# Kernel optimization log

Measured on AMD Instinct MI355X. Metric: run time of the kernel, lower is better.

## Reference

```python
import jax, jax.numpy as jnp
import numpy as np
from jax import lax

B, CIN, COUT, H, W = 8, 256, 256, 96, 96


def _conv_bn(x, w, g, b, act):
    # 3x3 conv, stride 1, SAME padding (NCHW / OIHW), then per-channel affine (folded BN)
    y = lax.conv_general_dilated(x, w, (1, 1), 'SAME',
                                 dimension_numbers=('NCHW', 'OIHW', 'NCHW'))
    y = y * g[None, :, None, None] + b[None, :, None, None]
    return jax.nn.relu(y) if act else y


def setup_inputs() -> dict:
    key = jax.random.key(0)
    ks = jax.random.split(key, 16)
    def wgt(k, cout, cin):
        return jax.random.normal(k, (cout, cin, 3, 3), jnp.float32) * (1.0 / np.sqrt(cin * 9))
    def gb(k, c):
        k1, k2 = jax.random.split(k)
        return (1.0 + 0.1 * jax.random.normal(k1, (c,), jnp.float32),
                0.1 * jax.random.normal(k2, (c,), jnp.float32))
    g_p1, b_p1 = gb(ks[1], COUT); g_p2, b_p2 = gb(ks[3], COUT)
    g_p, b_p = gb(ks[5], COUT); g_c1, b_c1 = gb(ks[7], COUT); g_c2, b_c2 = gb(ks[9], COUT)
    return {
        'x': jax.random.normal(ks[0], (B, CIN, H, W), jnp.float32),
        'w_p1': wgt(ks[10], COUT, CIN), 'g_p1': g_p1, 'b_p1': b_p1,
        'w_p2': wgt(ks[11], COUT, CIN), 'g_p2': g_p2, 'b_p2': b_p2,
        'w_p': wgt(ks[12], COUT, COUT), 'g_p': g_p, 'b_p': b_p,
        'w_c1': wgt(ks[13], COUT, CIN), 'g_c1': g_c1, 'b_c1': b_c1,
        'w_c2': wgt(ks[14], COUT, COUT), 'g_c2': g_c2, 'b_c2': b_c2,
    }


def reference(x, w_p1, g_p1, b_p1, w_p2, g_p2, b_p2, w_p, g_p, b_p,
              w_c1, g_c1, b_c1, w_c2, g_c2, b_c2):
    # branch 1: conv -> TopPool (cummax up, i.e. reverse along H) -> BottomPool (cummax down)
    p1 = _conv_bn(x, w_p1, g_p1, b_p1, act=True)
    pool1 = lax.cummax(p1, axis=2, reverse=True)   # TopPool
    pool1 = lax.cummax(pool1, axis=2)              # BottomPool
    # branch 2: conv -> LeftPool (reverse along W) -> RightPool
    p2 = _conv_bn(x, w_p2, g_p2, b_p2, act=True)
    pool2 = lax.cummax(p2, axis=3, reverse=True)   # LeftPool
    pool2 = lax.cummax(pool2, axis=3)              # RightPool
    p_conv = _conv_bn(pool1 + pool2, w_p, g_p, b_p, act=False)
    conv1 = _conv_bn(x, w_c1, g_c1, b_c1, act=False)
    relu = jax.nn.relu(p_conv + conv1)
    return _conv_bn(relu, w_c2, g_c2, b_c2, act=True)
```

## Files before the change

### kernel.cpp

```cpp
#include <hip/hip_runtime.h>


typedef _Float16 f16x8 __attribute__((ext_vector_type(8)));
typedef _Float16 f16x4v __attribute__((ext_vector_type(4)));
typedef float f32x4 __attribute__((ext_vector_type(4)));

#define HP 98
#define WP 98
#define KTOT 2304
#define WSET (256*KTOT)
#define XPAD_E ((size_t)8*HP*WP*256)
#define UVP_E  ((size_t)8*98*256)
#define UV2_E  ((size_t)3*8*96*256)
#define WUV_SET 196608

__device__ __forceinline__ int xcd_swz(int bid, int nwg)
{
  return (bid & 7) * (nwg >> 3) + (bid >> 3);
}

#define BUF_Q 24576
#define SMEM_Q 49152

struct CtxQ {
  unsigned goff[6];
  unsigned lds_stage;
  unsigned aoff;
  int wl, quad, wv;
  int b, h0, w0;
};

template<int SW>
__device__ __forceinline__ CtxQ make_ctxQ(int spatial, int ch)
{
  CtxQ c;
  c.b = spatial / 36;
  const int tt = spatial - c.b * 36;
  const int ht = tt / 6, wt = tt - ht * 6;
  c.h0 = ht * 16; c.w0 = wt * 16;
  const int tid = threadIdx.x, lane = tid & 63;
  c.wv = tid >> 6;
  c.quad = lane >> 4; c.wl = lane & 15;
  c.aoff = (unsigned)((ch * 8 + c.wv * 2) * 512 + c.wl * 32 + c.quad * 8);
  const unsigned base_hw = (unsigned)(c.b * HP + c.h0) * WP + c.w0;
#pragma unroll
  for (int t = 0; t < 6; ++t) {
    int s = (c.wv * 6 + t) * 16 + (lane >> 2);
    if (s > 323) s = 323;
    const int x = s / 18, y = s - x * 18;
    const int wh = SW ? y : x, ww = SW ? x : y;
    c.goff[t] = (base_hw + (unsigned)(wh * WP + ww)) * 256u + (lane & 3) * 8u;
  }
  c.lds_stage = (unsigned)(c.wv * 6) * 1024u + (unsigned)lane * 16u;
  return c;
}

__device__ __forceinline__ void stage_cbQ(const _Float16* __restrict__ src,
                                          char* sbuf, const CtxQ& c, int buf, int cb)
{
  char* l0 = sbuf + buf * BUF_Q + c.lds_stage;
#pragma unroll
  for (int t = 0; t < 6; ++t) {
    const _Float16* g = src + c.goff[t] + cb * 32;
    __builtin_amdgcn_global_load_lds(
        (const __attribute__((address_space(1))) void*)g,
        (__attribute__((address_space(3))) void*)(l0 + t * 1024), 16, 0, 0);
  }
}

template<int TR>
__device__ __forceinline__ void conv_accumQ(const _Float16* __restrict__ src,
                                            const _Float16* __restrict__ wkb,
                                            char* sbuf, const CtxQ& c, f32x4 acc[2][16])
{
  const _Float16* A0 = wkb + c.aoff;
  stage_cbQ(src, sbuf, c, 0, 0);
#pragma unroll 1
  for (int cb = 0; cb < 8; ++cb) {
    __syncthreads();
    if (cb < 7) stage_cbQ(src, sbuf, c, (cb + 1) & 1, cb + 1);
    const _Float16* B = (const _Float16*)(sbuf + (cb & 1) * BUF_Q);
    const _Float16* A = A0 + cb * (9 * 8192);
#pragma unroll
    for (int o = 0; o < 3; ++o) {
      f16x8 af[3][2];
#pragma unroll
      for (int p = 0; p < 3; ++p) {
        const int tap = (TR == 0) ? p * 3 + o : o * 3 + p;
#pragma unroll
        for (int i = 0; i < 2; ++i)
          af[p][i] = *(const f16x8*)(A + tap * 8192 + i * 512);
      }
#pragma unroll
      for (int jh = 0; jh < 2; ++jh) {
        f16x8 cache[10];
#pragma unroll
        for (int r = 0; r < 10; ++r)
          cache[r] = *(const f16x8*)(B + ((jh * 8 + r) * 18 + c.wl + o) * 32 + c.quad * 8);
#pragma unroll
        for (int p = 0; p < 3; ++p)
#pragma unroll
          for (int i = 0; i < 2; ++i)
#pragma unroll
            for (int j = 0; j < 8; ++j)
              acc[i][jh * 8 + j] = __builtin_amdgcn_mfma_f32_16x16x32_f16(
                  af[p][i], cache[j + p], acc[i][jh * 8 + j], 0, 0, 0);
      }
    }
  }
  __syncthreads();
}

#define ZERO_ACCQ(acc) \
  _Pragma("unroll") for (int i = 0; i < 2; ++i) \
  _Pragma("unroll") for (int j = 0; j < 16; ++j) acc[i][j] = (f32x4){0.f,0.f,0.f,0.f};

__global__ __launch_bounds__(256, 2) void k_conv_p12(
    const _Float16* __restrict__ xpad, const _Float16* __restrict__ wk,
    const float* __restrict__ bias1, const float* __restrict__ bias2,
    float* __restrict__ u_pad, float* __restrict__ v_pad)
{
  __shared__ __align__(16) char smem[SMEM_Q];
  const int lin = xcd_swz(blockIdx.x, 1152);
  const int set = lin >= 576;
  const int rem = lin - set * 576;
  const int spatial = rem >> 1, ch = rem & 1;
  f32x4 acc[2][16];
  ZERO_ACCQ(acc)
  if (set == 0) {
    CtxQ c = make_ctxQ<0>(spatial, ch);
    conv_accumQ<0>(xpad, wk, smem, c, acc);
#pragma unroll
    for (int i = 0; i < 2; ++i) {
      const int co = (ch * 8 + c.wv * 2 + i) * 16 + c.quad * 4;
      const float4 bs = *(const float4*)(bias1 + co);
      float m0 = 0.f, m1 = 0.f, m2 = 0.f, m3 = 0.f;
#pragma unroll
      for (int j = 0; j < 16; ++j) {
        m0 = fmaxf(m0, acc[i][j][0] + bs.x);
        m1 = fmaxf(m1, acc[i][j][1] + bs.y);
        m2 = fmaxf(m2, acc[i][j][2] + bs.z);
        m3 = fmaxf(m3, acc[i][j][3] + bs.w);
      }
      unsigned* tgt = (unsigned*)(u_pad + ((size_t)c.b * 98 + (c.w0 + c.wl + 1)) * 256 + co);
      atomicMax(tgt + 0, __float_as_uint(m0));
      atomicMax(tgt + 1, __float_as_uint(m1));
      atomicMax(tgt + 2, __float_as_uint(m2));
      atomicMax(tgt + 3, __float_as_uint(m3));
    }
  } else {
    CtxQ c = make_ctxQ<1>(spatial, ch);
    conv_accumQ<1>(xpad, wk + WSET, smem, c, acc);
#pragma unroll
    for (int i = 0; i < 2; ++i) {
      const int co = (ch * 8 + c.wv * 2 + i) * 16 + c.quad * 4;
      const float4 bs = *(const float4*)(bias2 + co);
      float m0 = 0.f, m1 = 0.f, m2 = 0.f, m3 = 0.f;
#pragma unroll
      for (int j = 0; j < 16; ++j) {
        m0 = fmaxf(m0, acc[i][j][0] + bs.x);
        m1 = fmaxf(m1, acc[i][j][1] + bs.y);
        m2 = fmaxf(m2, acc[i][j][2] + bs.z);
        m3 = fmaxf(m3, acc[i][j][3] + bs.w);
      }
      unsigned* tgt = (unsigned*)(v_pad + ((size_t)c.b * 98 + (c.h0 + c.wl + 1)) * 256 + co);
      atomicMax(tgt + 0, __float_as_uint(m0));
      atomicMax(tgt + 1, __float_as_uint(m1));
      atomicMax(tgt + 2, __float_as_uint(m2));
      atomicMax(tgt + 3, __float_as_uint(m3));
    }
  }
}

__global__ __launch_bounds__(256, 2) void k_uv1d(
    const float* __restrict__ u_pad, const float* __restrict__ v_pad,
    const _Float16* __restrict__ wuv, float* __restrict__ u2, float* __restrict__ v2)
{
  const int id = blockIdx.x;
  const int b = id & 7, cs = (id >> 3) % 3, t = id / 24;
  const float* src = t ? v_pad : u_pad;
  float* dst = t ? v2 : u2;
  const _Float16* A0 = wuv + (size_t)(t * 3 + cs) * WUV_SET;
  const int lane = threadIdx.x & 63, wv = threadIdx.x >> 6;
  const int quad = lane >> 4, l16 = lane & 15;

  f32x4 acc[4][6];
#pragma unroll
  for (int i = 0; i < 4; ++i)
#pragma unroll
    for (int j = 0; j < 6; ++j) acc[i][j] = (f32x4){0.f, 0.f, 0.f, 0.f};

#pragma unroll 1
  for (int kb = 0; kb < 24; ++kb) {
    const int dw = kb >> 3, cb = kb & 7;
    f16x8 bf[6];
#pragma unroll
    for (int j = 0; j < 6; ++j) {
      const int pos = j * 16 + l16;
      const float* p = src + ((size_t)b * 98 + (pos + dw)) * 256 + cb * 32 + quad * 8;
      const float4 x0 = *(const float4*)p;
      const float4 x1 = *(const float4*)(p + 4);
      f16x8 v;
      v[0] = (_Float16)x0.x; v[1] = (_Float16)x0.y; v[2] = (_Float16)x0.z; v[3] = (_Float16)x0.w;
      v[4] = (_Float16)x1.x; v[5] = (_Float16)x1.y; v[6] = (_Float16)x1.z; v[7] = (_Float16)x1.w;
      bf[j] = v;
    }
    f16x8 af[4];
#pragma unroll
    for (int i = 0; i < 4; ++i)
      af[i] = *(const f16x8*)(A0 + (size_t)(kb * 16 + wv * 4 + i) * 512 + l16 * 32 + quad * 8);
#pragma unroll
    for (int i = 0; i < 4; ++i)
#pragma unroll
      for (int j = 0; j < 6; ++j)
        acc[i][j] = __builtin_amdgcn_mfma_f32_16x16x32_f16(af[i], bf[j], acc[i][j], 0, 0, 0);
  }
#pragma unroll
  for (int i = 0; i < 4; ++i)
#pragma unroll
    for (int j = 0; j < 6; ++j) {
      const int pos = j * 16 + l16;
      const int co = wv * 64 + i * 16 + quad * 4;
      *(f32x4*)(dst + ((size_t)(cs * 8 + b) * 96 + pos) * 256 + co) = acc[i][j];
    }
}

__global__ __launch_bounds__(256, 2) void k_conv_c1f(
    const _Float16* __restrict__ xpad, const _Float16* __restrict__ wkc1,
    const float* __restrict__ bias_p, const float* __restrict__ bias_c1,
    const float* __restrict__ u2, const float* __restrict__ v2,
    _Float16* __restrict__ rpad)
{
  __shared__ __align__(16) char smem[SMEM_Q];
  const int lin = xcd_swz(blockIdx.x, 576);
  const int spatial = lin >> 1, ch = lin & 1;
  CtxQ c = make_ctxQ<0>(spatial, ch);
  f32x4 acc[2][16];
  ZERO_ACCQ(acc)
  conv_accumQ<0>(xpad, wkc1, smem, c, acc);

  const int w = c.w0 + c.wl;
  const int wcase = (w == 0) ? 0 : ((w == 95) ? 2 : 1);
#pragma unroll
  for (int i = 0; i < 2; ++i) {
    const int co = (ch * 8 + c.wv * 2 + i) * 16 + c.quad * 4;
    float4 bs = *(const float4*)(bias_p + co);
    const float4 b2 = *(const float4*)(bias_c1 + co);
    bs.x += b2.x; bs.y += b2.y; bs.z += b2.z; bs.w += b2.w;
#pragma unroll
    for (int j = 0; j < 16; ++j) {
      const int h = c.h0 + j;
      const int hcase = (h == 0) ? 0 : ((h == 95) ? 2 : 1);
      const float4 uq = *(const float4*)(u2 + ((size_t)(hcase * 8 + c.b) * 96 + w) * 256 + co);
      const float4 vq = *(const float4*)(v2 + ((size_t)(wcase * 8 + c.b) * 96 + h) * 256 + co);
      f16x4v pk;
      pk[0] = (_Float16)fmaxf(acc[i][j][0] + bs.x + uq.x + vq.x, 0.f);
      pk[1] = (_Float16)fmaxf(acc[i][j][1] + bs.y + uq.y + vq.y, 0.f);
      pk[2] = (_Float16)fmaxf(acc[i][j][2] + bs.z + uq.z + vq.z, 0.f);
      pk[3] = (_Float16)fmaxf(acc[i][j][3] + bs.w + uq.w + vq.w, 0.f);
      *(f16x4v*)(rpad + ((size_t)(c.b * HP + h + 1) * WP + w + 1) * 256 + co) = pk;
    }
  }
}

__global__ __launch_bounds__(256, 2) void k_conv_c2(
    const _Float16* __restrict__ rpad, const _Float16* __restrict__ wkc2,
    const float* __restrict__ bias, float* __restrict__ dout)
{
  __shared__ __align__(16) char smem[SMEM_Q];
  const int lin = xcd_swz(blockIdx.x, 576);
  const int spatial = lin >> 1, ch = lin & 1;
  CtxQ c = make_ctxQ<0>(spatial, ch);
  f32x4 acc[2][16];
  ZERO_ACCQ(acc)
  conv_accumQ<0>(rpad, wkc2, smem, c, acc);

  const int w = c.w0 + c.wl;
#pragma unroll
  for (int j = 0; j < 16; ++j) {
    const int h = c.h0 + j;
    float* op = dout + (size_t)c.b * 2359296 + h * 96 + w;
#pragma unroll
    for (int i = 0; i < 2; ++i) {
      const int co = (ch * 8 + c.wv * 2 + i) * 16 + c.quad * 4;
      const float4 bs = *(const float4*)(bias + co);
      op[(size_t)(co + 0) * 9216] = fmaxf(acc[i][j][0] + bs.x, 0.f);
      op[(size_t)(co + 1) * 9216] = fmaxf(acc[i][j][1] + bs.y, 0.f);
      op[(size_t)(co + 2) * 9216] = fmaxf(acc[i][j][2] + bs.z, 0.f);
      op[(size_t)(co + 3) * 9216] = fmaxf(acc[i][j][3] + bs.w, 0.f);
    }
  }
}

__global__ void k_border(_Float16* __restrict__ xpad, _Float16* __restrict__ rpad)
{
  const int idx = blockIdx.x, b = blockIdx.y;
  _Float16* buf = blockIdx.z ? rpad : xpad;
  int h, w;
  if (idx < 98)       { h = 0;  w = idx; }
  else if (idx < 196) { h = 97; w = idx - 98; }
  else { const int r = idx - 196; h = 1 + (r >> 1); w = (r & 1) ? 97 : 0; }
  buf[((size_t)(b * HP + h) * WP + w) * 256 + threadIdx.x] = (_Float16)0.f;
}

__global__ void k_pack_x(const float* __restrict__ x, _Float16* __restrict__ xpad)
{
  __shared__ float tile[32][33];
  const int bh = blockIdx.x;
  const int b = bh / 96, h = bh - b * 96;
  const int c0 = blockIdx.y * 32, w0 = blockIdx.z * 32;
  const int tx = threadIdx.x & 31, ty = threadIdx.x >> 5;
#pragma unroll
  for (int i = 0; i < 4; ++i) {
    int cI = c0 + ty + i * 8;
    tile[ty + i * 8][tx] = x[(((size_t)b * 256 + cI) * 96 + h) * 96 + w0 + tx];
  }
  __syncthreads();
#pragma unroll
  for (int i = 0; i < 4; ++i) {
    int w = w0 + ty + i * 8;
    xpad[((size_t)(b * HP + h + 1) * WP + (w + 1)) * 256 + c0 + tx] =
        (_Float16)tile[tx][ty + i * 8];
  }
}

__global__ void k_repack_w(const float* w0, const float* g0, const float* w1, const float* g1,
                           const float* w2, const float* g2, const float* w3, const float* g3,
                           const float* w4, const float* g4, _Float16* __restrict__ wk)
{
  const int set = blockIdx.y;
  const float* w; const float* g;
  switch (set) {
    case 0: w = w0; g = g0; break;
    case 1: w = w1; g = g1; break;
    case 2: w = w2; g = g2; break;
    case 3: w = w3; g = g3; break;
    default: w = w4; g = g4; break;
  }
  const int t = blockIdx.x * 256 + threadIdx.x;
  const int co = t >> 8, ci = t & 255;
  const int cb = ci >> 5, kk = ci & 31, cog = co >> 4, m = co & 15;
  const float gv = g[co];
  const float* src = w + ((size_t)co * 256 + ci) * 9;
  _Float16* dst = wk + (size_t)set * WSET + cog * 512 + m * 32 + kk;
#pragma unroll
  for (int tap = 0; tap < 9; ++tap)
    dst[(cb * 9 + tap) * 8192] = (_Float16)(src[tap] * gv);
}

__global__ void k_repack_uvw(const float* __restrict__ wp, const float* __restrict__ gp,
                             _Float16* __restrict__ wuv)
{
  const int tcs = blockIdx.y;
  const int tt = tcs / 3, cs = tcs - tt * 3;
  const int idx = blockIdx.x * 256 + threadIdx.x;
  const int co = idx >> 8, ci = idx & 255;
  const float gv = gp[co];
  const float* src = wp + ((size_t)co * 256 + ci) * 9;
  const int lo = (cs == 0) ? 1 : 0, hi = (cs == 2) ? 1 : 2;
  _Float16* base = wuv + (size_t)tcs * WUV_SET;
#pragma unroll
  for (int d = 0; d < 3; ++d) {
    float s = 0.f;
    for (int e = lo; e <= hi; ++e)
      s += (tt == 0) ? src[e * 3 + d] : src[d * 3 + e];
    const int k = d * 256 + ci;
    const int kb = k >> 5, kk = k & 31;
    base[(size_t)(kb * 16 + (co >> 4)) * 512 + (co & 15) * 32 + kk] = (_Float16)(s * gv);
  }
}

extern "C" void kernel_launch(void* const* d_in, const int* in_sizes, int n_in,
                              void* d_out, int out_size, void* d_ws, size_t ws_size,
                              hipStream_t stream)
{
  const float* x    = (const float*)d_in[0];
  const float* w_p1 = (const float*)d_in[1];
  const float* g_p1 = (const float*)d_in[2];
  const float* b_p1 = (const float*)d_in[3];
  const float* w_p2 = (const float*)d_in[4];
  const float* g_p2 = (const float*)d_in[5];
  const float* b_p2 = (const float*)d_in[6];
  const float* w_p  = (const float*)d_in[7];
  const float* g_p  = (const float*)d_in[8];
  const float* b_p  = (const float*)d_in[9];
  const float* w_c1 = (const float*)d_in[10];
  const float* g_c1 = (const float*)d_in[11];
  const float* b_c1 = (const float*)d_in[12];
  const float* w_c2 = (const float*)d_in[13];
  const float* g_c2 = (const float*)d_in[14];
  const float* b_c2 = (const float*)d_in[15];

  char* ws = (char*)d_ws;
  size_t off = 0;
  _Float16* x_pad = (_Float16*)(ws + off); off += XPAD_E * 2;
  _Float16* r_pad = (_Float16*)(ws + off); off += XPAD_E * 2;
  _Float16* wks   = (_Float16*)(ws + off); off += (size_t)5 * WSET * 2;
  _Float16* wuv   = (_Float16*)(ws + off); off += (size_t)6 * WUV_SET * 2;
  float*    u_pad = (float*)(ws + off);    off += UVP_E * 4;
  float*    v_pad = (float*)(ws + off);    off += UVP_E * 4;
  float*    u2    = (float*)(ws + off);    off += UV2_E * 4;
  float*    v2    = (float*)(ws + off);    off += UV2_E * 4;
  (void)ws_size; (void)in_sizes; (void)n_in; (void)out_size;

  hipMemsetAsync(u_pad, 0, UVP_E * 4, stream);
  hipMemsetAsync(v_pad, 0, UVP_E * 4, stream);

  k_border    <<<dim3(388, 8, 2), 256, 0, stream>>>(x_pad, r_pad);
  k_pack_x    <<<dim3(768, 8, 3), 256, 0, stream>>>(x, x_pad);
  k_repack_w  <<<dim3(256, 5),    256, 0, stream>>>(w_p1, g_p1, w_p2, g_p2, w_p, g_p,
                                                    w_c1, g_c1, w_c2, g_c2, wks);
  k_repack_uvw<<<dim3(256, 6),    256, 0, stream>>>(w_p, g_p, wuv);
  k_conv_p12  <<<1152, 256, 0, stream>>>(x_pad, wks, b_p1, b_p2, u_pad, v_pad);
  k_uv1d      <<<48,   256, 0, stream>>>(u_pad, v_pad, wuv, u2, v2);
  k_conv_c1f  <<<576,  256, 0, stream>>>(x_pad, wks + (size_t)3 * WSET, b_p, b_c1,
                                         u2, v2, r_pad);
  k_conv_c2   <<<576,  256, 0, stream>>>(r_pad, wks + (size_t)4 * WSET, b_c2,
                                         (float*)d_out);
}
```

Baseline: 555.7 us.

## Halve conv workgroup size to 2 waves with 64-channel slices; split uv1d over positions

```diff
diff --git a/kernel.cpp b/kernel.cpp
--- a/kernel.cpp
+++ b/kernel.cpp
@@ -24,6 +24,7 @@
 
 struct CtxQ {
   unsigned goff[6];
+  unsigned mask;
   unsigned lds_stage;
   unsigned aoff;
   int wl, quad, wv;
@@ -41,23 +42,29 @@
   const int tid = threadIdx.x, lane = tid & 63;
   c.wv = tid >> 6;
   c.quad = lane >> 4; c.wl = lane & 15;
-  c.aoff = (unsigned)((ch * 8 + c.wv * 2) * 512 + c.wl * 32 + c.quad * 8);
+  c.aoff = (unsigned)((ch * 4 + c.wv * 2) * 512 + c.wl * 32 + c.quad * 8);
   const unsigned base_hw = (unsigned)(c.b * HP + c.h0) * WP + c.w0;
+  const int lg = lane >> 2;
+  c.mask = 0;
 #pragma unroll
   for (int t = 0; t < 6; ++t) {
-    int s = (c.wv * 6 + t) * 16 + (lane >> 2);
-    if (s > 323) s = 323;
+    const int s = (c.wv * 12 + t) * 16 + lg;
     const int x = s / 18, y = s - x * 18;
     const int wh = SW ? y : x, ww = SW ? x : y;
     c.goff[t] = (base_hw + (unsigned)(wh * WP + ww)) * 256u + (lane & 3) * 8u;
-  }
-  c.lds_stage = (unsigned)(c.wv * 6) * 1024u + (unsigned)lane * 16u;
+    if (y >= 12) c.mask |= (1u << t);
+    if (s > 227) c.mask |= (1u << (6 + t));
+  }
+  c.lds_stage = (unsigned)(c.wv * 12) * 1024u + (unsigned)lane * 16u;
   return c;
 }
 
+template<int SW>
 __device__ __forceinline__ void stage_cbQ(const _Float16* __restrict__ src,
                                           char* sbuf, const CtxQ& c, int buf, int cb)
 {
+  constexpr int D0 = SW ? (6 * WP + 5) * 256 : (5 * WP + 6) * 256;
+  constexpr int D1 = SW ? (6 - 12 * WP) * 256 : (6 * WP - 12) * 256;
   char* l0 = sbuf + buf * BUF_Q + c.lds_stage;
 #pragma unroll
   for (int t = 0; t < 6; ++t) {
@@ -66,19 +73,28 @@
         (const __attribute__((address_space(1))) void*)g,
         (__attribute__((address_space(3))) void*)(l0 + t * 1024), 16, 0, 0);
   }
-}
-
-template<int TR>
+#pragma unroll
+  for (int t = 0; t < 6; ++t) {
+    const int d = ((c.mask >> (6 + t)) & 1) ? 0
+                : (((c.mask >> t) & 1) ? D1 : D0);
+    const _Float16* g = src + (int)(c.goff[t] + (unsigned)d) + cb * 32;
+    __builtin_amdgcn_global_load_lds(
+        (const __attribute__((address_space(1))) void*)g,
+        (__attribute__((address_space(3))) void*)(l0 + (6 + t) * 1024), 16, 0, 0);
+  }
+}
+
+template<int S>
 __device__ __forceinline__ void conv_accumQ(const _Float16* __restrict__ src,
                                             const _Float16* __restrict__ wkb,
                                             char* sbuf, const CtxQ& c, f32x4 acc[2][16])
 {
   const _Float16* A0 = wkb + c.aoff;
-  stage_cbQ(src, sbuf, c, 0, 0);
+  stage_cbQ<S>(src, sbuf, c, 0, 0);
 #pragma unroll 1
   for (int cb = 0; cb < 8; ++cb) {
     __syncthreads();
-    if (cb < 7) stage_cbQ(src, sbuf, c, (cb + 1) & 1, cb + 1);
+    if (cb < 7) stage_cbQ<S>(src, sbuf, c, (cb + 1) & 1, cb + 1);
     const _Float16* B = (const _Float16*)(sbuf + (cb & 1) * BUF_Q);
     const _Float16* A = A0 + cb * (9 * 8192);
 #pragma unroll
@@ -86,7 +102,7 @@
       f16x8 af[3][2];
 #pragma unroll
       for (int p = 0; p < 3; ++p) {
-        const int tap = (TR == 0) ? p * 3 + o : o * 3 + p;
+        const int tap = (S == 0) ? p * 3 + o : o * 3 + p;
 #pragma unroll
         for (int i = 0; i < 2; ++i)
           af[p][i] = *(const f16x8*)(A + tap * 8192 + i * 512);
@@ -115,16 +131,16 @@
   _Pragma("unroll") for (int i = 0; i < 2; ++i) \
   _Pragma("unroll") for (int j = 0; j < 16; ++j) acc[i][j] = (f32x4){0.f,0.f,0.f,0.f};
 
-__global__ __launch_bounds__(256, 2) void k_conv_p12(
+__global__ __launch_bounds__(128, 2) void k_conv_p12(
     const _Float16* __restrict__ xpad, const _Float16* __restrict__ wk,
     const float* __restrict__ bias1, const float* __restrict__ bias2,
     float* __restrict__ u_pad, float* __restrict__ v_pad)
 {
   __shared__ __align__(16) char smem[SMEM_Q];
-  const int lin = xcd_swz(blockIdx.x, 1152);
-  const int set = lin >= 576;
-  const int rem = lin - set * 576;
-  const int spatial = rem >> 1, ch = rem & 1;
+  const int lin = xcd_swz(blockIdx.x, 2304);
+  const int set = lin >= 1152;
+  const int rem = lin - set * 1152;
+  const int spatial = rem >> 2, ch = rem & 3;
   f32x4 acc[2][16];
   ZERO_ACCQ(acc)
   if (set == 0) {
@@ -132,7 +148,7 @@
     conv_accumQ<0>(xpad, wk, smem, c, acc);
 #pragma unroll
     for (int i = 0; i < 2; ++i) {
-      const int co = (ch * 8 + c.wv * 2 + i) * 16 + c.quad * 4;
+      const int co = (ch * 4 + c.wv * 2 + i) * 16 + c.quad * 4;
       const float4 bs = *(const float4*)(bias1 + co);
       float m0 = 0.f, m1 = 0.f, m2 = 0.f, m3 = 0.f;
 #pragma unroll
@@ -153,7 +169,7 @@
     conv_accumQ<1>(xpad, wk + WSET, smem, c, acc);
 #pragma unroll
     for (int i = 0; i < 2; ++i) {
-      const int co = (ch * 8 + c.wv * 2 + i) * 16 + c.quad * 4;
+      const int co = (ch * 4 + c.wv * 2 + i) * 16 + c.quad * 4;
       const float4 bs = *(const float4*)(bias2 + co);
       float m0 = 0.f, m1 = 0.f, m2 = 0.f, m3 = 0.f;
 #pragma unroll
@@ -177,6 +193,7 @@
     const _Float16* __restrict__ wuv, float* __restrict__ u2, float* __restrict__ v2)
 {
   const int id = blockIdx.x;
+  const int py = blockIdx.y;
   const int b = id & 7, cs = (id >> 3) % 3, t = id / 24;
   const float* src = t ? v_pad : u_pad;
   float* dst = t ? v2 : u2;
@@ -184,19 +201,19 @@
   const int lane = threadIdx.x & 63, wv = threadIdx.x >> 6;
   const int quad = lane >> 4, l16 = lane & 15;
 
-  f32x4 acc[4][6];
+  f32x4 acc[4][3];
 #pragma unroll
   for (int i = 0; i < 4; ++i)
 #pragma unroll
-    for (int j = 0; j < 6; ++j) acc[i][j] = (f32x4){0.f, 0.f, 0.f, 0.f};
+    for (int j = 0; j < 3; ++j) acc[i][j] = (f32x4){0.f, 0.f, 0.f, 0.f};
 
 #pragma unroll 1
   for (int kb = 0; kb < 24; ++kb) {
     const int dw = kb >> 3, cb = kb & 7;
-    f16x8 bf[6];
-#pragma unroll
-    for (int j = 0; j < 6; ++j) {
-      const int pos = j * 16 + l16;
+    f16x8 bf[3];
+#pragma unroll
+    for (int j = 0; j < 3; ++j) {
+      const int pos = py * 48 + j * 16 + l16;
       const float* p = src + ((size_t)b * 98 + (pos + dw)) * 256 + cb * 32 + quad * 8;
       const float4 x0 = *(const float4*)p;
       const float4 x1 = *(const float4*)(p + 4);
@@ -212,28 +229,28 @@
 #pragma unroll
     for (int i = 0; i < 4; ++i)
 #pragma unroll
-      for (int j = 0; j < 6; ++j)
+      for (int j = 0; j < 3; ++j)
         acc[i][j] = __builtin_amdgcn_mfma_f32_16x16x32_f16(af[i], bf[j], acc[i][j], 0, 0, 0);
   }
 #pragma unroll
   for (int i = 0; i < 4; ++i)
 #pragma unroll
-    for (int j = 0; j < 6; ++j) {
-      const int pos = j * 16 + l16;
+    for (int j = 0; j < 3; ++j) {
+      const int pos = py * 48 + j * 16 + l16;
       const int co = wv * 64 + i * 16 + quad * 4;
       *(f32x4*)(dst + ((size_t)(cs * 8 + b) * 96 + pos) * 256 + co) = acc[i][j];
     }
 }
 
-__global__ __launch_bounds__(256, 2) void k_conv_c1f(
+__global__ __launch_bounds__(128, 2) void k_conv_c1f(
     const _Float16* __restrict__ xpad, const _Float16* __restrict__ wkc1,
     const float* __restrict__ bias_p, const float* __restrict__ bias_c1,
     const float* __restrict__ u2, const float* __restrict__ v2,
     _Float16* __restrict__ rpad)
 {
   __shared__ __align__(16) char smem[SMEM_Q];
-  const int lin = xcd_swz(blockIdx.x, 576);
-  const int spatial = lin >> 1, ch = lin & 1;
+  const int lin = xcd_swz(blockIdx.x, 1152);
+  const int spatial = lin >> 2, ch = lin & 3;
   CtxQ c = make_ctxQ<0>(spatial, ch);
   f32x4 acc[2][16];
   ZERO_ACCQ(acc)
@@ -243,7 +260,7 @@
   const int wcase = (w == 0) ? 0 : ((w == 95) ? 2 : 1);
 #pragma unroll
   for (int i = 0; i < 2; ++i) {
-    const int co = (ch * 8 + c.wv * 2 + i) * 16 + c.quad * 4;
+    const int co = (ch * 4 + c.wv * 2 + i) * 16 + c.quad * 4;
     float4 bs = *(const float4*)(bias_p + co);
     const float4 b2 = *(const float4*)(bias_c1 + co);
     bs.x += b2.x; bs.y += b2.y; bs.z += b2.z; bs.w += b2.w;
@@ -263,13 +280,13 @@
   }
 }
 
-__global__ __launch_bounds__(256, 2) void k_conv_c2(
+__global__ __launch_bounds__(128, 2) void k_conv_c2(
     const _Float16* __restrict__ rpad, const _Float16* __restrict__ wkc2,
     const float* __restrict__ bias, float* __restrict__ dout)
 {
   __shared__ __align__(16) char smem[SMEM_Q];
-  const int lin = xcd_swz(blockIdx.x, 576);
-  const int spatial = lin >> 1, ch = lin & 1;
+  const int lin = xcd_swz(blockIdx.x, 1152);
+  const int spatial = lin >> 2, ch = lin & 3;
   CtxQ c = make_ctxQ<0>(spatial, ch);
   f32x4 acc[2][16];
   ZERO_ACCQ(acc)
@@ -282,7 +299,7 @@
     float* op = dout + (size_t)c.b * 2359296 + h * 96 + w;
 #pragma unroll
     for (int i = 0; i < 2; ++i) {
-      const int co = (ch * 8 + c.wv * 2 + i) * 16 + c.quad * 4;
+      const int co = (ch * 4 + c.wv * 2 + i) * 16 + c.quad * 4;
       const float4 bs = *(const float4*)(bias + co);
       op[(size_t)(co + 0) * 9216] = fmaxf(acc[i][j][0] + bs.x, 0.f);
       op[(size_t)(co + 1) * 9216] = fmaxf(acc[i][j][1] + bs.y, 0.f);
@@ -411,10 +428,10 @@
   k_repack_w  <<<dim3(256, 5),    256, 0, stream>>>(w_p1, g_p1, w_p2, g_p2, w_p, g_p,
                                                     w_c1, g_c1, w_c2, g_c2, wks);
   k_repack_uvw<<<dim3(256, 6),    256, 0, stream>>>(w_p, g_p, wuv);
-  k_conv_p12  <<<1152, 256, 0, stream>>>(x_pad, wks, b_p1, b_p2, u_pad, v_pad);
-  k_uv1d      <<<48,   256, 0, stream>>>(u_pad, v_pad, wuv, u2, v2);
-  k_conv_c1f  <<<576,  256, 0, stream>>>(x_pad, wks + (size_t)3 * WSET, b_p, b_c1,
+  k_conv_p12  <<<2304, 128, 0, stream>>>(x_pad, wks, b_p1, b_p2, u_pad, v_pad);
+  k_uv1d      <<<dim3(48, 2), 256, 0, stream>>>(u_pad, v_pad, wuv, u2, v2);
+  k_conv_c1f  <<<1152, 128, 0, stream>>>(x_pad, wks + (size_t)3 * WSET, b_p, b_c1,
                                          u2, v2, r_pad);
-  k_conv_c2   <<<576,  256, 0, stream>>>(r_pad, wks + (size_t)4 * WSET, b_c2,
+  k_conv_c2   <<<1152, 128, 0, stream>>>(r_pad, wks + (size_t)4 * WSET, b_c2,
                                          (float*)d_out);
 }
```

Result: no change. 549.9 us (-1.1%).
